# Performance work log

Hardware: AMD Instinct MI355X
Metric: run time of the kernel (lower is better)

The kernel has to match this reference:

```python
import jax, jax.numpy as jnp
import numpy as np

KM_ITERS = 25  # fixed Lloyd iterations (original kmeans_pytorch iterates to tol; fixed count for jit)
EPS = 1e-12    # torch F.normalize clamp_min eps


def l2_normalize(x):
    n = jnp.sqrt(jnp.sum(x * x, axis=1, keepdims=True))
    return x / jnp.maximum(n, EPS)


def kmeans(X, k, iters=KM_ITERS):
    """Lloyd's algorithm, euclidean distance, deterministic init from first k rows."""
    N = X.shape[0]
    centers0 = X[:k]
    xsq = jnp.sum(X * X, axis=1, keepdims=True)  # [N,1]

    def dist2(centers):
        # squared euclidean distances [N,k]; argmin identical to euclidean
        return xsq - 2.0 * (X @ centers.T) + jnp.sum(centers * centers, axis=1)

    def step(i, centers):
        lab = jnp.argmin(dist2(centers), axis=1)  # [N]
        sums = jax.ops.segment_sum(X, lab, num_segments=k)  # [k,d]
        cnts = jax.ops.segment_sum(jnp.ones((N,), X.dtype), lab, num_segments=k)  # [k]
        new = sums / jnp.maximum(cnts, 1.0)[:, None]
        # keep old center for empty clusters
        return jnp.where(cnts[:, None] > 0, new, centers)

    centers = jax.lax.fori_loop(0, iters, step, centers0)
    labels = jnp.argmin(dist2(centers), axis=1)
    return labels, centers


def setup_inputs() -> dict:
    key = jax.random.key(0)
    ks = jax.random.split(key, 8)
    N, D, H, K = 50000, 1024, 512, 64
    x = jax.random.normal(ks[0], (N, D), dtype=jnp.float32)
    xw = jax.random.normal(ks[1], (N, D), dtype=jnp.float32)
    s1 = 1.0 / np.sqrt(D)
    s2 = 1.0 / np.sqrt(H)
    W1 = jax.random.uniform(ks[2], (D, H), jnp.float32, -s1, s1)
    b1 = jax.random.uniform(ks[3], (H,), jnp.float32, -s1, s1)
    W2 = jax.random.uniform(ks[4], (D, H), jnp.float32, -s1, s1)
    b2 = jax.random.uniform(ks[5], (H,), jnp.float32, -s1, s1)
    Wc = jax.random.uniform(ks[6], (H, K), jnp.float32, -s2, s2)
    bc = jax.random.uniform(ks[7], (K,), jnp.float32, -s2, s2)
    return {"x": x, "xw": xw, "W1": W1, "b1": b1, "W2": W2, "b2": b2,
            "Wc": Wc, "bc": bc, "n_clusters": K}


def reference(x, xw, W1, b1, W2, b2, Wc, bc, n_clusters):
    out1 = l2_normalize(x @ W1 + b1)   # layers1 + F.normalize(dim=1)
    out2 = l2_normalize(xw @ W2 + b2)  # layers2 + F.normalize(dim=1)
    # kmeans results are detached in the original (converted to numpy)
    km_label, km_centers = kmeans(jax.lax.stop_gradient(out2), n_clusters)
    u1 = jax.nn.softmax(out1 @ Wc + bc, axis=1)
    u2 = jax.nn.softmax(out2 @ Wc + bc, axis=1)
    return (out1, out2, km_label, km_centers, u1, u2)
```

## Files before the change

### kernel.cpp

```cpp
#include <hip/hip_runtime.h>
#include <math.h>

#define ND 1024
#define HID 512
#define KCL 64
#define KM_ITERS 25
#define CHSZ 256


__device__ __forceinline__ float np_pw512_sq(const float* __restrict__ a, int lane)
{
#pragma clang fp contract(off)
  float r = 0.f;
  if (lane < 32) {
    const float* blk = a + 128 * (lane >> 3);
    int j = lane & 7;
    float t = blk[j];
    r = t * t;
#pragma unroll
    for (int i = 8; i < 128; i += 8) { float u = blk[j + i]; r = r + u * u; }
  }
  float t1 = r  + __shfl_xor(r,  1);
  float t2 = t1 + __shfl_xor(t1, 2);
  float t3 = t2 + __shfl_xor(t2, 4);
  float u4 = t3 + __shfl_xor(t3, 8);
  float v5 = u4 + __shfl_xor(u4, 16);
  return __shfl(v5, 0);
}

__global__ __launch_bounds__(512) void np_gemm2_kernel(
    const float* __restrict__ A, const float* __restrict__ W,
    const float* __restrict__ bias, float* __restrict__ C)
{
#pragma clang fp contract(off)
  __shared__ float4 As4[16 * 256];
  const int t = threadIdx.x;
  const size_t r0 = (size_t)blockIdx.x * 16;
  const float4* Ag = (const float4*)(A + r0 * ND);
  for (int i = t; i < 16 * 256; i += 512) As4[i] = Ag[i];
  __syncthreads();

  float s1[16], s2[16], s3[16], s4[16];
#pragma unroll
  for (int r = 0; r < 16; r++) { s1[r] = 0.f; s2[r] = 0.f; s3[r] = 0.f; s4[r] = 0.f; }

#define G2_STEP(ACC, K4)                                          \
  {                                                               \
    const int k = (K4) * 4;                                       \
    float w0 = W[(size_t)(k + 0) * HID + t];                      \
    float w1 = W[(size_t)(k + 1) * HID + t];                      \
    float w2 = W[(size_t)(k + 2) * HID + t];                      \
    float w3 = W[(size_t)(k + 3) * HID + t];                      \
    _Pragma("unroll")                                             \
    for (int r = 0; r < 16; r++) {                                \
      float4 a = As4[r * 256 + (K4)];                             \
      float s = ACC[r];                                           \
      s = fmaf(a.x, w0, s);                                       \
      s = fmaf(a.y, w1, s);                                       \
      s = fmaf(a.z, w2, s);                                       \
      s = fmaf(a.w, w3, s);                                       \
      ACC[r] = s;                                                 \
    }                                                             \
  }

#pragma unroll 2
  for (int k4 = 0; k4 < 80; k4++)    G2_STEP(s1, k4)
#pragma unroll 2
  for (int k4 = 80; k4 < 160; k4++)  G2_STEP(s2, k4)
#pragma unroll 2
  for (int k4 = 160; k4 < 208; k4++) G2_STEP(s3, k4)
#pragma unroll 2
  for (int k4 = 208; k4 < 256; k4++) G2_STEP(s4, k4)
#undef G2_STEP

  float b = bias[t];
#pragma unroll
  for (int r = 0; r < 16; r++)
    C[(r0 + r) * HID + t] = (((s1[r] + s2[r]) + s3[r]) + s4[r]) + b;
}

__global__ __launch_bounds__(256) void np_rownorm_xsq_kernel(
    float* __restrict__ M, float* __restrict__ xsq, int N)
{
#pragma clang fp contract(off)
  __shared__ float sy[4][512];
  int w = threadIdx.x >> 6, lane = threadIdx.x & 63;
  int r = blockIdx.x * 4 + w;
  if (r >= N) return;
  float* row = M + (size_t)r * HID;
  float s = np_pw512_sq(row, lane);
  float n = fmaxf((float)sqrt((double)s), 1e-12f);
#pragma unroll
  for (int j = 0; j < 8; j++) {
    float y = row[lane * 8 + j] / n;
    row[lane * 8 + j] = y;
    sy[w][lane * 8 + j] = y;
  }
  __syncthreads();
  float s2 = np_pw512_sq(sy[w], lane);
  if (lane == 0) xsq[r] = s2;
}

__global__ __launch_bounds__(64) void np_csqT_kernel(
    const float* __restrict__ cen, float* __restrict__ csq, float* __restrict__ Ct4f)
{
#pragma clang fp contract(off)
  int c = blockIdx.x;
  int lane = threadIdx.x;
  const float* row = cen + (size_t)c * HID;
  float s = np_pw512_sq(row, lane);
  if (lane == 0) csq[c] = s;
  for (int k = lane; k < HID; k += 64)
    Ct4f[((size_t)(k >> 2) * KCL + c) * 4 + (k & 3)] = row[k];
}

__global__ __launch_bounds__(256) void np_label_kernel(
    const float* __restrict__ X, const float4* __restrict__ Ct4,
    const float* __restrict__ xsq, const float* __restrict__ csq,
    int* __restrict__ lab, int N)
{
#pragma clang fp contract(off)
  __shared__ float4 Xs4[16 * 128];
  const int t = threadIdx.x;
  const int p0 = blockIdx.x * 16;
  const float4* Xg = (const float4*)(X + (size_t)p0 * HID);
  for (int i = t; i < 16 * 128; i += 256) Xs4[i] = Xg[i];
  __syncthreads();

  const int w = t >> 6, c = t & 63;
  const int pb = w * 4 * 128;
  float s0[4], s1[4];
#pragma unroll
  for (int pt = 0; pt < 4; pt++) { s0[pt] = 0.f; s1[pt] = 0.f; }

#pragma unroll 4
  for (int k4 = 0; k4 < 64; k4++) {
    float4 ct = Ct4[(size_t)k4 * KCL + c];
#pragma unroll
    for (int pt = 0; pt < 4; pt++) {
      float4 xq = Xs4[pb + pt * 128 + k4];
      float s = s0[pt];
      s = fmaf(xq.x, ct.x, s);
      s = fmaf(xq.y, ct.y, s);
      s = fmaf(xq.z, ct.z, s);
      s = fmaf(xq.w, ct.w, s);
      s0[pt] = s;
    }
  }
#pragma unroll 4
  for (int k4 = 64; k4 < 128; k4++) {
    float4 ct = Ct4[(size_t)k4 * KCL + c];
#pragma unroll
    for (int pt = 0; pt < 4; pt++) {
      float4 xq = Xs4[pb + pt * 128 + k4];
      float s = s1[pt];
      s = fmaf(xq.x, ct.x, s);
      s = fmaf(xq.y, ct.y, s);
      s = fmaf(xq.z, ct.z, s);
      s = fmaf(xq.w, ct.w, s);
      s1[pt] = s;
    }
  }

#pragma unroll
  for (int pt = 0; pt < 4; pt++) {
    int p = p0 + (w * 4 + pt);
    float dot = s0[pt] + s1[pt];
    float t2 = 2.0f * dot;
    float u = xsq[p] - t2;
    float sc = u + csq[c];
    float bv = sc; int bi = c;
#pragma unroll
    for (int m = 32; m; m >>= 1) {
      float ov = __shfl_xor(bv, m);
      int   oi = __shfl_xor(bi, m);
      if (ov < bv || (ov == bv && oi < bi)) { bv = ov; bi = oi; }
    }
    if (c == 0 && p < N) lab[p] = bi;
  }
}


__global__ __launch_bounds__(256) void k_count(
    const int* __restrict__ lab, int* __restrict__ cntch, int N)
{
  int ch = blockIdx.x;
  int p = ch * CHSZ + threadIdx.x;
  int l = (p < N) ? lab[p] : -1;
  int w = threadIdx.x >> 6, lane = threadIdx.x & 63;
  __shared__ int wc[4][64];
  for (int cc = 0; cc < 64; cc++) {
    unsigned long long mm = __ballot(l == cc);
    if (lane == cc) wc[w][cc] = __popcll(mm);
  }
  __syncthreads();
  if (threadIdx.x < 64) {
    int cc = threadIdx.x;
    cntch[ch * 64 + cc] = wc[0][cc] + wc[1][cc] + wc[2][cc] + wc[3][cc];
  }
}

__global__ __launch_bounds__(64) void k_prefix(
    const int* __restrict__ cntch, int* __restrict__ off,
    int* __restrict__ base, int* __restrict__ cnt, int CH)
{
  int c = threadIdx.x;
  int run = 0;
#pragma unroll 8
  for (int ch = 0; ch < CH; ch++) { off[ch * 64 + c] = run; run += cntch[ch * 64 + c]; }
  cnt[c] = run;
  __shared__ int tot[64];
  tot[c] = run;
  __syncthreads();
  if (c == 0) {
    int b = 0;
    for (int cc = 0; cc < 64; cc++) { base[cc] = b; b += tot[cc]; }
  }
  __syncthreads();
  int b = base[c];
#pragma unroll 8
  for (int ch = 0; ch < CH; ch++) off[ch * 64 + c] += b;
}

__global__ __launch_bounds__(256) void k_scatter(
    const int* __restrict__ lab, const int* __restrict__ off,
    int* __restrict__ list, int N)
{
  int ch = blockIdx.x;
  int p = ch * CHSZ + threadIdx.x;
  int l = (p < N) ? lab[p] : -1;
  int w = threadIdx.x >> 6, lane = threadIdx.x & 63;
  __shared__ int wc[4][64];
  int rank = 0;
  for (int cc = 0; cc < 64; cc++) {
    unsigned long long mm = __ballot(l == cc);
    if (lane == cc) wc[w][cc] = __popcll(mm);
    if (l == cc) rank = __popcll(mm & ((1ull << lane) - 1ull));
  }
  __syncthreads();
  if (p < N) {
    int before = 0;
    for (int ww = 0; ww < 4; ww++) if (ww < w) before += wc[ww][l];
    list[off[ch * 64 + l] + before + rank] = p;
  }
}

__global__ __launch_bounds__(512) void np_seg_update_kernel(
    const float* __restrict__ X, const int* __restrict__ list,
    const int* __restrict__ base, const int* __restrict__ cnt,
    float* __restrict__ cen, float* __restrict__ csq, float* __restrict__ Ct4f)
{
#pragma clang fp contract(off)
  __shared__ float row[512];
  const int c = blockIdx.x;
  const int d = threadIdx.x;
  const int n = cnt[c];
  const int* lp = list + base[c];
  float s = 0.f;
  int i = 0;
  for (; i + 8 <= n; i += 8) {
    int p0 = lp[i + 0], p1 = lp[i + 1], p2 = lp[i + 2], p3 = lp[i + 3];
    int p4 = lp[i + 4], p5 = lp[i + 5], p6 = lp[i + 6], p7 = lp[i + 7];
    float x0 = X[(size_t)p0 * HID + d];
    float x1 = X[(size_t)p1 * HID + d];
    float x2 = X[(size_t)p2 * HID + d];
    float x3 = X[(size_t)p3 * HID + d];
    float x4 = X[(size_t)p4 * HID + d];
    float x5 = X[(size_t)p5 * HID + d];
    float x6 = X[(size_t)p6 * HID + d];
    float x7 = X[(size_t)p7 * HID + d];
    s = s + x0; s = s + x1; s = s + x2; s = s + x3;
    s = s + x4; s = s + x5; s = s + x6; s = s + x7;
  }
  for (; i < n; i++) s = s + X[(size_t)lp[i] * HID + d];

  float v;
  if (n > 0) {
    v = s / fmaxf((float)n, 1.0f);
    cen[(size_t)c * HID + d] = v;
  } else {
    v = cen[(size_t)c * HID + d];
  }
  row[d] = v;
  __syncthreads();
  if (d < 64) {
    float sq = np_pw512_sq(row, d);
    if (d == 0) csq[c] = sq;
  }
  Ct4f[((size_t)(d >> 2) * KCL + c) * 4 + (d & 3)] = v;
}

__global__ void copy_f32_kernel(const float* __restrict__ s, float* __restrict__ d, int n)
{
  int i = blockIdx.x * blockDim.x + threadIdx.x;
  if (i < n) d[i] = s[i];
}
__global__ void lab_to_f32_kernel(const int* __restrict__ s, float* __restrict__ d, int n)
{
  int i = blockIdx.x * blockDim.x + threadIdx.x;
  if (i < n) d[i] = (float)s[i];
}


__global__ __launch_bounds__(256) void rownorm_kernel(float* __restrict__ M, int N)
{
  int r = blockIdx.x * 4 + (threadIdx.x >> 6);
  int lane = threadIdx.x & 63;
  if (r >= N) return;
  float* row = M + (size_t)r * HID;
  float4 v0 = *reinterpret_cast<const float4*>(&row[lane * 8]);
  float4 v1 = *reinterpret_cast<const float4*>(&row[lane * 8 + 4]);
  float s = v0.x*v0.x + v0.y*v0.y + v0.z*v0.z + v0.w*v0.w
          + v1.x*v1.x + v1.y*v1.y + v1.z*v1.z + v1.w*v1.w;
#pragma unroll
  for (int off = 32; off; off >>= 1) s += __shfl_xor(s, off);
  float nrm = fmaxf(sqrtf(s), 1e-12f);
  v0.x /= nrm; v0.y /= nrm; v0.z /= nrm; v0.w /= nrm;
  v1.x /= nrm; v1.y /= nrm; v1.z /= nrm; v1.w /= nrm;
  *reinterpret_cast<float4*>(&row[lane * 8]) = v0;
  *reinterpret_cast<float4*>(&row[lane * 8 + 4]) = v1;
}

__global__ __launch_bounds__(256) void clf_softmax_kernel(
    const float* __restrict__ X, const float* __restrict__ W,
    const float* __restrict__ bias, float* __restrict__ U, int N)
{
  int p = blockIdx.x * 4 + (threadIdx.x >> 6);
  int c = threadIdx.x & 63;
  if (p >= N) return;
  const float* xr = X + (size_t)p * HID;
  float acc = 0.f;
  for (int d = 0; d < HID; d++) acc = fmaf(xr[d], W[(size_t)d * KCL + c], acc);
  float l = acc + bias[c];
  float mx = l;
#pragma unroll
  for (int m = 32; m; m >>= 1) mx = fmaxf(mx, __shfl_xor(mx, m));
  float e = expf(l - mx);
  float s = e;
#pragma unroll
  for (int m = 32; m; m >>= 1) s += __shfl_xor(s, m);
  U[(size_t)p * KCL + c] = e / s;
}

extern "C" void kernel_launch(void* const* d_in, const int* in_sizes, int n_in,
                              void* d_out, int out_size, void* d_ws, size_t ws_size,
                              hipStream_t stream)
{
  const float* x  = (const float*)d_in[0];
  const float* xw = (const float*)d_in[1];
  const float* W1 = (const float*)d_in[2];
  const float* b1 = (const float*)d_in[3];
  const float* W2 = (const float*)d_in[4];
  const float* b2 = (const float*)d_in[5];
  const float* Wc = (const float*)d_in[6];
  const float* bc = (const float*)d_in[7];

  const int N = in_sizes[0] / ND;
  float* out  = (float*)d_out;
  float* out1 = out;
  float* out2 = out1 + (size_t)N * HID;
  float* labf = out2 + (size_t)N * HID;
  float* cenf = labf + N;
  float* u1   = cenf + (size_t)KCL * HID;
  float* u2   = u1 + (size_t)N * KCL;

  const int CH = (N + CHSZ - 1) / CHSZ;

  float* cen   = u2;
  float* Ct4f  = cen + KCL * HID;
  float* csq   = Ct4f + 128 * KCL * 4;
  float* xsq   = csq + KCL;
  int*   cnt   = (int*)(xsq + N);
  int*   lab   = cnt + KCL;
  int*   list  = lab + N;
  int*   cntch = list + N;
  int*   off   = cntch + CH * 64;
  int*   base  = off + CH * 64;
  const float4* Ct4 = (const float4*)Ct4f;

  const int pblocks = (N + 3) / 4;
  const int gblocks = N / 16;
  const int lblocks = (N + 15) / 16;

  np_gemm2_kernel<<<gblocks, 512, 0, stream>>>(xw, W2, b2, out2);
  np_rownorm_xsq_kernel<<<pblocks, 256, 0, stream>>>(out2, xsq, N);
  copy_f32_kernel<<<(KCL * HID + 255) / 256, 256, 0, stream>>>(out2, cen, KCL * HID);
  np_csqT_kernel<<<KCL, 64, 0, stream>>>(cen, csq, Ct4f);

  for (int it = 0; it < KM_ITERS; ++it) {
    np_label_kernel<<<lblocks, 256, 0, stream>>>(out2, Ct4, xsq, csq, lab, N);
    k_count<<<CH, 256, 0, stream>>>(lab, cntch, N);
    k_prefix<<<1, 64, 0, stream>>>(cntch, off, base, cnt, CH);
    k_scatter<<<CH, 256, 0, stream>>>(lab, off, list, N);
    np_seg_update_kernel<<<KCL, 512, 0, stream>>>(out2, list, base, cnt, cen, csq, Ct4f);
  }
  np_label_kernel<<<lblocks, 256, 0, stream>>>(out2, Ct4, xsq, csq, lab, N);

  lab_to_f32_kernel<<<(N + 255) / 256, 256, 0, stream>>>(lab, labf, N);
  copy_f32_kernel<<<(KCL * HID + 255) / 256, 256, 0, stream>>>(cen, cenf, KCL * HID);

  np_gemm2_kernel<<<gblocks, 512, 0, stream>>>(x, W1, b1, out1);
  rownorm_kernel<<<pblocks, 256, 0, stream>>>(out1, N);
  clf_softmax_kernel<<<pblocks, 256, 0, stream>>>(out1, Wc, bc, u1, N);
  clf_softmax_kernel<<<pblocks, 256, 0, stream>>>(out2, Wc, bc, u2, N);
}
```

Before: 8.693 ms.

## Replace LDS staging with direct wave-uniform global loads in GEMM and label kernels

Removes the shared-memory staging of input rows and the barrier in both the projection GEMM and the k-means labeling kernel. Each wave instead reads its rows straight from global memory through wave-uniform pointers, which readfirstlane scalarizes so the loads can go through the scalar path. The labeling kernel also doubles the points per wave from 4 to 8, halving the block count to reuse each center load across more points. The cost is more register pressure and a reliance on the scalar cache or broadcast global loads keeping up, where LDS reads were cheap before.

Result: slower. 14.08 ms (+62.0%).

```diff
diff --git a/kernel.cpp b/kernel.cpp
--- a/kernel.cpp
+++ b/kernel.cpp
@@ -28,39 +28,43 @@
   return __shfl(v5, 0);
 }
 
+__device__ __forceinline__ const float* scalarize_ptr(const float* p)
+{
+  uint64_t ap = (uint64_t)(uintptr_t)p;
+  uint32_t lo = __builtin_amdgcn_readfirstlane((uint32_t)ap);
+  uint32_t hi = __builtin_amdgcn_readfirstlane((uint32_t)(ap >> 32));
+  return (const float*)(uintptr_t)(((uint64_t)hi << 32) | lo);
+}
+
 __global__ __launch_bounds__(512) void np_gemm2_kernel(
     const float* __restrict__ A, const float* __restrict__ W,
     const float* __restrict__ bias, float* __restrict__ C)
 {
 #pragma clang fp contract(off)
-  __shared__ float4 As4[16 * 256];
   const int t = threadIdx.x;
   const size_t r0 = (size_t)blockIdx.x * 16;
-  const float4* Ag = (const float4*)(A + r0 * ND);
-  for (int i = t; i < 16 * 256; i += 512) As4[i] = Ag[i];
-  __syncthreads();
-
+  const float* a0p = A + r0 * ND;
   float s1[16], s2[16], s3[16], s4[16];
 #pragma unroll
   for (int r = 0; r < 16; r++) { s1[r] = 0.f; s2[r] = 0.f; s3[r] = 0.f; s4[r] = 0.f; }
 
-#define G2_STEP(ACC, K4)                                          \
-  {                                                               \
-    const int k = (K4) * 4;                                       \
-    float w0 = W[(size_t)(k + 0) * HID + t];                      \
-    float w1 = W[(size_t)(k + 1) * HID + t];                      \
-    float w2 = W[(size_t)(k + 2) * HID + t];                      \
-    float w3 = W[(size_t)(k + 3) * HID + t];                      \
-    _Pragma("unroll")                                             \
-    for (int r = 0; r < 16; r++) {                                \
-      float4 a = As4[r * 256 + (K4)];                             \
-      float s = ACC[r];                                           \
-      s = fmaf(a.x, w0, s);                                       \
-      s = fmaf(a.y, w1, s);                                       \
-      s = fmaf(a.z, w2, s);                                       \
-      s = fmaf(a.w, w3, s);                                       \
-      ACC[r] = s;                                                 \
-    }                                                             \
+#define G2_STEP(ACC, K4)                                                       \
+  {                                                                            \
+    const int k = (K4) * 4;                                                    \
+    float w0 = W[(size_t)(k + 0) * HID + t];                                   \
+    float w1 = W[(size_t)(k + 1) * HID + t];                                   \
+    float w2 = W[(size_t)(k + 2) * HID + t];                                   \
+    float w3 = W[(size_t)(k + 3) * HID + t];                                   \
+    _Pragma("unroll")                                                          \
+    for (int r = 0; r < 16; r++) {                                             \
+      float4 a = *reinterpret_cast<const float4*>(a0p + (size_t)r * ND + k);   \
+      float s = ACC[r];                                                        \
+      s = fmaf(a.x, w0, s);                                                    \
+      s = fmaf(a.y, w1, s);                                                    \
+      s = fmaf(a.z, w2, s);                                                    \
+      s = fmaf(a.w, w3, s);                                                    \
+      ACC[r] = s;                                                              \
+    }                                                                          \
   }
 
 #pragma unroll 2
@@ -120,25 +124,25 @@
     int* __restrict__ lab, int N)
 {
 #pragma clang fp contract(off)
-  __shared__ float4 Xs4[16 * 128];
   const int t = threadIdx.x;
-  const int p0 = blockIdx.x * 16;
-  const float4* Xg = (const float4*)(X + (size_t)p0 * HID);
-  for (int i = t; i < 16 * 128; i += 256) Xs4[i] = Xg[i];
-  __syncthreads();
-
   const int w = t >> 6, c = t & 63;
-  const int pb = w * 4 * 128;
-  float s0[4], s1[4];
-#pragma unroll
-  for (int pt = 0; pt < 4; pt++) { s0[pt] = 0.f; s1[pt] = 0.f; }
-
-#pragma unroll 4
+  const int p0 = blockIdx.x * 32 + w * 8;
+  const float* xp[8];
+#pragma unroll
+  for (int pt = 0; pt < 8; pt++) {
+    int p = p0 + pt; if (p >= N) p = N - 1;
+    xp[pt] = scalarize_ptr(X + (size_t)p * HID);
+  }
+  float s0[8], s1[8];
+#pragma unroll
+  for (int pt = 0; pt < 8; pt++) { s0[pt] = 0.f; s1[pt] = 0.f; }
+
+#pragma unroll 2
   for (int k4 = 0; k4 < 64; k4++) {
     float4 ct = Ct4[(size_t)k4 * KCL + c];
 #pragma unroll
-    for (int pt = 0; pt < 4; pt++) {
-      float4 xq = Xs4[pb + pt * 128 + k4];
+    for (int pt = 0; pt < 8; pt++) {
+      float4 xq = *reinterpret_cast<const float4*>(xp[pt] + k4 * 4);
       float s = s0[pt];
       s = fmaf(xq.x, ct.x, s);
       s = fmaf(xq.y, ct.y, s);
@@ -147,12 +151,12 @@
       s0[pt] = s;
     }
   }
-#pragma unroll 4
+#pragma unroll 2
   for (int k4 = 64; k4 < 128; k4++) {
     float4 ct = Ct4[(size_t)k4 * KCL + c];
 #pragma unroll
-    for (int pt = 0; pt < 4; pt++) {
-      float4 xq = Xs4[pb + pt * 128 + k4];
+    for (int pt = 0; pt < 8; pt++) {
+      float4 xq = *reinterpret_cast<const float4*>(xp[pt] + k4 * 4);
       float s = s1[pt];
       s = fmaf(xq.x, ct.x, s);
       s = fmaf(xq.y, ct.y, s);
@@ -163,11 +167,12 @@
   }
 
 #pragma unroll
-  for (int pt = 0; pt < 4; pt++) {
-    int p = p0 + (w * 4 + pt);
+  for (int pt = 0; pt < 8; pt++) {
+    int p = p0 + pt;
+    int pc = (p < N) ? p : N - 1;
     float dot = s0[pt] + s1[pt];
     float t2 = 2.0f * dot;
-    float u = xsq[p] - t2;
+    float u = xsq[pc] - t2;
     float sc = u + csq[c];
     float bv = sc; int bi = c;
 #pragma unroll
@@ -380,7 +385,7 @@
 
   const int pblocks = (N + 3) / 4;
   const int gblocks = N / 16;
-  const int lblocks = (N + 15) / 16;
+  const int lblocks = (N + 31) / 32;
 
   np_gemm2_kernel<<<gblocks, 512, 0, stream>>>(xw, W2, b2, out2);
   np_rownorm_xsq_kernel<<<pblocks, 256, 0, stream>>>(out2, xsq, N);
```
